# Optimization experiments

Hardware: AMD Instinct MI355X
Metric: run time of the kernel (lower is better)

## Reference

```python
import jax, jax.numpy as jnp
import numpy as np

N = 4096
FIN = 256
FOUT = 256
H = 1  # num_heads MUST be 1: edge projections reshape [N,N,H] -> (1,N,N)
NEG_MASK = -1000000.0
LRELU_SLOPE = 0.2
ESP = 1e-06
LN_EPS = 1e-05


def setup_inputs() -> dict:
    key = jax.random.key(0)
    ks = jax.random.split(key, 9)
    nodes_features = jax.random.normal(ks[0], (N, FIN), dtype=jnp.float32)
    degree_matrix = jax.random.normal(ks[1], (N, N), dtype=jnp.float32)
    edges_features_distance = jax.random.uniform(ks[2], (N, N), dtype=jnp.float32)
    edges_features_bond = jax.random.uniform(ks[3], (N, N), dtype=jnp.float32)
    # learned parameters (xavier-ish scale)
    proj_param = jax.random.normal(ks[4], (H, FIN, FOUT), dtype=jnp.float32) * (1.0 / np.sqrt(FIN))
    a_src = jax.random.normal(ks[5], (H, FOUT, 1), dtype=jnp.float32) * (1.0 / np.sqrt(FOUT))
    a_tgt = jax.random.normal(ks[6], (H, FOUT, 1), dtype=jnp.float32) * (1.0 / np.sqrt(FOUT))
    w_dist = jax.random.normal(ks[7], (H, 1), dtype=jnp.float32)  # nn.Linear(1, H).weight
    w_bond = jax.random.normal(ks[8], (H, 1), dtype=jnp.float32)
    return {
        "nodes_features": nodes_features,
        "degree_matrix": degree_matrix,
        "edges_features_distance": edges_features_distance,
        "edges_features_bond": edges_features_bond,
        "proj_param": proj_param,
        "a_src": a_src,
        "a_tgt": a_tgt,
        "w_dist": w_dist,
        "w_bond": w_bond,
        "cutoff": 0,
    }


def reference(nodes_features, degree_matrix, edges_features_distance,
              edges_features_bond, proj_param, a_src, a_tgt, w_dist, w_bond,
              cutoff=0):
    n = nodes_features.shape[0]
    h, fin, fout = proj_param.shape
    # connectivity mask: keep degree where positive, else large negative
    connectivity_mask = jnp.where(degree_matrix > 0, degree_matrix, NEG_MASK)
    # node projection: [H, N, Fout] (dropout is identity in eval)
    proj = jnp.einsum('nf,hfo->hno', nodes_features, proj_param)
    # attention scores: outer-sum of per-node source/target scores
    s_src = jnp.einsum('hno,hoi->hni', proj, a_src)      # [H, N, 1]
    s_tgt = jnp.einsum('hno,hoi->hni', proj, a_tgt)      # [H, N, 1]
    all_scores = jax.nn.leaky_relu(s_src + jnp.swapaxes(s_tgt, 1, 2), LRELU_SLOPE)  # [H,N,N]
    # edge contributions: Linear(1, H) on scalar edge features, reshaped (1,N,N) (H==1)
    dist_c = ((-edges_features_distance)[..., None] * w_dist[:, 0]).reshape(1, n, n)
    bond_c = (edges_features_bond[..., None] * w_bond[:, 0]).reshape(1, n, n)
    all_scores = all_scores + dist_c + bond_c
    # masked softmax over neighbors
    attn = jax.nn.softmax(all_scores + connectivity_mask[None], axis=-1)  # [H,N,N]
    # weighted aggregation
    out = jnp.einsum('hnm,hmo->hno', attn, proj)  # [H, N, Fout]
    # faithful to torch: transpose(2,1) -> [H,Fout,N] then contiguous view(-1,H,Fout)
    out = jnp.transpose(out, (0, 2, 1)).reshape(-1, h, fout)
    # concat heads (skip connection and bias are disabled per init args)
    out = out.reshape(-1, h * fout)
    out = jax.nn.elu(out)  # ELU activation, alpha=1
    # ---- no_grad connectivity update ----
    o = jax.lax.stop_gradient(out)
    dm = jax.lax.stop_gradient(degree_matrix)
    sim = o @ o.T                                        # [N, N]
    decay = -jax.lax.stop_gradient(edges_features_distance)
    upd = jax.nn.sigmoid(sim) * decay * (dm > 0).astype(o.dtype)
    upd = upd + ESP
    mean = jnp.mean(upd, axis=-1, keepdims=True)
    var = jnp.mean(jnp.square(upd - mean), axis=-1, keepdims=True)
    upd = (upd - mean) / jnp.sqrt(var + LN_EPS)          # layer_norm, no affine
    upd = upd + upd.T
    return out, upd
```

## Files before the change

kernel.cpp:

```cpp
#include <hip/hip_runtime.h>


using f32x4  = __attribute__((ext_vector_type(4))) float;
using bf16x8 = __attribute__((ext_vector_type(8))) __bf16;
using bf16x4 = __attribute__((ext_vector_type(4))) __bf16;
using u32x4  = __attribute__((ext_vector_type(4))) unsigned int;

__global__ __launch_bounds__(256) void cvt_nodes_kernel(const float* __restrict__ x,
                                                        __bf16* __restrict__ y) {
  int i = (blockIdx.x * 256 + threadIdx.x) * 4;
  f32x4 v = *(const f32x4*)(x + i);
  bf16x4 o = { (__bf16)v[0], (__bf16)v[1], (__bf16)v[2], (__bf16)v[3] };
  *(bf16x4*)(y + i) = o;
}

__global__ __launch_bounds__(256) void cvt_wt_kernel(const float* __restrict__ w,
                                                     __bf16* __restrict__ wt) {
  int i = blockIdx.x * 256 + threadIdx.x;
  int o = i >> 8, f = i & 255;
  wt[i] = (__bf16)w[f * 256 + o];
}

__global__ __launch_bounds__(256) void zero_kernel(float* __restrict__ p) {
  p[blockIdx.x * 256 + threadIdx.x] = 0.0f;
}

template<int BM, int BN, int MODE>
__global__ __launch_bounds__(256) void gemm_bf16_kernel(
    const __bf16* __restrict__ A, const __bf16* __restrict__ Bt,
    int M, int N, int K,
    float* __restrict__ outf, __bf16* __restrict__ outb,
    const float* __restrict__ e0, const float* __restrict__ e1,
    const __bf16* __restrict__ axp, float* __restrict__ outt)
{
  constexpr int LDT = 72;
  constexpr int MI = BM / 32;
  constexpr int NI = BN / 32;
  __shared__ alignas(16) __bf16 As[BM * LDT];
  __shared__ alignas(16) __bf16 Bs[BN * LDT];
  const int tid  = threadIdx.x;
  const int lane = tid & 63;
  const int wid  = tid >> 6;
  const int wm0  = (wid >> 1) * (BM / 2);
  const int wn0  = (wid & 1) * (BN / 2);
  const int m0   = blockIdx.x * BM;
  const int n0   = blockIdx.y * BN;
  const int lr   = lane & 15;
  const int lk   = lane >> 4;

  f32x4 acc[MI][NI];
#pragma unroll
  for (int a = 0; a < MI; ++a)
#pragma unroll
    for (int b = 0; b < NI; ++b) acc[a][b] = (f32x4){0.f, 0.f, 0.f, 0.f};

  for (int kt = 0; kt < K; kt += 64) {
    __syncthreads();
    for (int idx = tid; idx < BM * 8; idx += 256) {
      int r = idx >> 3, c = idx & 7;
      u32x4 v = *(const u32x4*)(A + (size_t)(m0 + r) * K + kt + c * 8);
      *(u32x4*)(As + r * LDT + c * 8) = v;
    }
    for (int idx = tid; idx < BN * 8; idx += 256) {
      int r = idx >> 3, c = idx & 7;
      u32x4 v = *(const u32x4*)(Bt + (size_t)(n0 + r) * K + kt + c * 8);
      *(u32x4*)(Bs + r * LDT + c * 8) = v;
    }
    __syncthreads();
#pragma unroll
    for (int kk = 0; kk < 2; ++kk) {
      bf16x8 av[MI], bv[NI];
#pragma unroll
      for (int mi = 0; mi < MI; ++mi)
        av[mi] = *(const bf16x8*)(As + (wm0 + mi * 16 + lr) * LDT + kk * 32 + lk * 8);
#pragma unroll
      for (int ni = 0; ni < NI; ++ni)
        bv[ni] = *(const bf16x8*)(Bs + (wn0 + ni * 16 + lr) * LDT + kk * 32 + lk * 8);
#pragma unroll
      for (int mi = 0; mi < MI; ++mi)
#pragma unroll
        for (int ni = 0; ni < NI; ++ni)
          acc[mi][ni] = __builtin_amdgcn_mfma_f32_16x16x32_bf16(av[mi], bv[ni], acc[mi][ni], 0, 0, 0);
    }
  }

#pragma unroll
  for (int mi = 0; mi < MI; ++mi) {
#pragma unroll
    for (int ni = 0; ni < NI; ++ni) {
#pragma unroll
      for (int j = 0; j < 4; ++j) {
        const int m = m0 + wm0 + mi * 16 + lk * 4 + j;
        const int n = n0 + wn0 + ni * 16 + lr;
        const float v = acc[mi][ni][j];
        if constexpr (MODE == 0) {
          outf[(size_t)m * 256 + n] = v;
          outb[(size_t)n * 4096 + m] = (__bf16)v;
        } else if constexpr (MODE == 2) {
          const size_t idx = (size_t)m * 4096 + n;
          const float d = e0[idx];
          const float g = e1[idx];
          const float s = 1.0f / (1.0f + expf(-v));
          outt[idx] = s * (-d) * (g > 0.f ? 1.0f : 0.0f) + 1e-6f;
        } else {
          const size_t idx = (size_t)m * 4096 + n;
          const float a = (float)axp[idx];
          const float s = 1.0f / (1.0f + expf(-v));
          outt[idx] = s * a + 1e-6f;
        }
      }
    }
  }
}

__global__ __launch_bounds__(256) void score_exp_kernel(
    const float* __restrict__ dist, const float* __restrict__ bond,
    const float* __restrict__ deg,  const float* __restrict__ ssrc,
    const float* __restrict__ stgt, const float* __restrict__ wdp,
    const float* __restrict__ wbp,  __bf16* __restrict__ P,
    __bf16* __restrict__ aux,       float* __restrict__ Lrow)
{
  const float wd = wdp[0], wb = wbp[0];
  const int lane = threadIdx.x & 63;
  size_t i = ((size_t)blockIdx.x * 256 + threadIdx.x) * 4;
  const size_t stride = (size_t)2048 * 256 * 4;
#pragma unroll 2
  for (int it = 0; it < 8; ++it, i += stride) {
    const int row = (int)(i >> 12);
    const int col = (int)(i & 4095);
    f32x4 d  = *(const f32x4*)(dist + i);
    f32x4 g  = *(const f32x4*)(deg + i);
    f32x4 b  = *(const f32x4*)(bond + i);
    f32x4 st = *(const f32x4*)(stgt + col);
    const float si = ssrc[row];
    f32x4 p;
    bf16x4 pb, ab;
#pragma unroll
    for (int q = 0; q < 4; ++q) {
      float x = si + st[q];
      x = x > 0.f ? x : 0.2f * x;
      x += -d[q] * wd + b[q] * wb + (g[q] > 0.f ? g[q] : -1000000.0f);
      p[q] = expf(x);
      pb[q] = (__bf16)p[q];
      ab[q] = (__bf16)(g[q] > 0.f ? -d[q] : 0.0f);
    }
    *(bf16x4*)(P + i) = pb;
    if (aux) *(bf16x4*)(aux + i) = ab;
    float s = p[0] + p[1] + p[2] + p[3];
#pragma unroll
    for (int o = 32; o; o >>= 1) s += __shfl_xor(s, o, 64);
    if (lane == 0) atomicAdd(Lrow + row, s);
  }
}

__global__ __launch_bounds__(256) void gemm_splitk_kernel(
    const __bf16* __restrict__ A, const __bf16* __restrict__ Bt,
    float* __restrict__ partial)
{
  constexpr int LDT = 72;
  __shared__ alignas(16) __bf16 As[64 * LDT];
  __shared__ alignas(16) __bf16 Bs[64 * LDT];
  const int tid  = threadIdx.x;
  const int lane = tid & 63;
  const int wid  = tid >> 6;
  const int wm0  = (wid >> 1) * 32;
  const int wn0  = (wid & 1) * 32;
  const int m0   = blockIdx.x * 64;
  const int n0   = blockIdx.y * 64;
  const int s    = blockIdx.z;
  const int lr   = lane & 15;
  const int lk   = lane >> 4;

  f32x4 acc[2][2];
#pragma unroll
  for (int a = 0; a < 2; ++a)
#pragma unroll
    for (int b = 0; b < 2; ++b) acc[a][b] = (f32x4){0.f, 0.f, 0.f, 0.f};

  const int k0 = s * 512;
  for (int kt = k0; kt < k0 + 512; kt += 64) {
    __syncthreads();
    for (int idx = tid; idx < 512; idx += 256) {
      int r = idx >> 3, c = idx & 7;
      u32x4 v = *(const u32x4*)(A + (size_t)(m0 + r) * 4096 + kt + c * 8);
      *(u32x4*)(As + r * LDT + c * 8) = v;
    }
    for (int idx = tid; idx < 512; idx += 256) {
      int r = idx >> 3, c = idx & 7;
      u32x4 v = *(const u32x4*)(Bt + (size_t)(n0 + r) * 4096 + kt + c * 8);
      *(u32x4*)(Bs + r * LDT + c * 8) = v;
    }
    __syncthreads();
#pragma unroll
    for (int kk = 0; kk < 2; ++kk) {
      bf16x8 av[2], bv[2];
#pragma unroll
      for (int mi = 0; mi < 2; ++mi)
        av[mi] = *(const bf16x8*)(As + (wm0 + mi * 16 + lr) * LDT + kk * 32 + lk * 8);
#pragma unroll
      for (int ni = 0; ni < 2; ++ni)
        bv[ni] = *(const bf16x8*)(Bs + (wn0 + ni * 16 + lr) * LDT + kk * 32 + lk * 8);
#pragma unroll
      for (int mi = 0; mi < 2; ++mi)
#pragma unroll
        for (int ni = 0; ni < 2; ++ni)
          acc[mi][ni] = __builtin_amdgcn_mfma_f32_16x16x32_bf16(av[mi], bv[ni], acc[mi][ni], 0, 0, 0);
    }
  }

  float* Pp = partial + (size_t)s * (4096 * 256);
#pragma unroll
  for (int mi = 0; mi < 2; ++mi)
#pragma unroll
    for (int ni = 0; ni < 2; ++ni)
#pragma unroll
      for (int j = 0; j < 4; ++j) {
        const int m = m0 + wm0 + mi * 16 + lk * 4 + j;
        const int n = n0 + wn0 + ni * 16 + lr;
        Pp[(size_t)m * 256 + n] = acc[mi][ni][j];
      }
}

__global__ __launch_bounds__(256) void reduce_elu_kernel(
    const float* __restrict__ partial, const float* __restrict__ Lrow,
    float* __restrict__ out0, __bf16* __restrict__ E)
{
  __shared__ float tile[64][65];
  __shared__ float invL[64];
  const int tid = threadIdx.x;
  const int m0 = blockIdx.x * 64;
  const int f0 = blockIdx.y * 64;
  if (tid < 64) invL[tid] = 1.0f / Lrow[m0 + tid];
  f32x4 accv[4];
#pragma unroll
  for (int i = 0; i < 4; ++i) {
    int lin = i * 1024 + tid * 4;
    int r = lin >> 6, c = lin & 63;
    f32x4 sum = (f32x4){0.f, 0.f, 0.f, 0.f};
#pragma unroll
    for (int s = 0; s < 8; ++s)
      sum += *(const f32x4*)(partial + (size_t)s * (4096 * 256) +
                             (size_t)(m0 + r) * 256 + f0 + c);
    accv[i] = sum;
  }
  __syncthreads();
#pragma unroll
  for (int i = 0; i < 4; ++i) {
    int lin = i * 1024 + tid * 4;
    int r = lin >> 6, c = lin & 63;
    const float inv = invL[r];
    tile[r][c]     = accv[i][0] * inv;
    tile[r][c + 1] = accv[i][1] * inv;
    tile[r][c + 2] = accv[i][2] * inv;
    tile[r][c + 3] = accv[i][3] * inv;
  }
  __syncthreads();
#pragma unroll
  for (int i = 0; i < 4; ++i) {
    int lin = i * 1024 + tid * 4;
    int rr = lin >> 6, cc = lin & 63;
    f32x4 e;
#pragma unroll
    for (int q = 0; q < 4; ++q) {
      float v = tile[cc + q][rr];
      e[q] = v > 0.f ? v : expm1f(v);
    }
    size_t idx = (size_t)(f0 + rr) * 4096 + m0 + cc;
    *(f32x4*)(out0 + idx) = e;
    bf16x4 eb = { (__bf16)e[0], (__bf16)e[1], (__bf16)e[2], (__bf16)e[3] };
    *(bf16x4*)(E + idx) = eb;
  }
}

__global__ __launch_bounds__(256) void sproj_kernel(const float* __restrict__ proj,
                                                    const float* __restrict__ asrc,
                                                    const float* __restrict__ atgt,
                                                    float* __restrict__ ssrc,
                                                    float* __restrict__ stgt) {
  const int row  = blockIdx.x * 4 + (threadIdx.x >> 6);
  const int lane = threadIdx.x & 63;
  f32x4 p = *(const f32x4*)(proj + (size_t)row * 256 + lane * 4);
  f32x4 a = *(const f32x4*)(asrc + lane * 4);
  f32x4 b = *(const f32x4*)(atgt + lane * 4);
  float d1 = p[0]*a[0] + p[1]*a[1] + p[2]*a[2] + p[3]*a[3];
  float d2 = p[0]*b[0] + p[1]*b[1] + p[2]*b[2] + p[3]*b[3];
#pragma unroll
  for (int o = 32; o; o >>= 1) { d1 += __shfl_xor(d1, o, 64); d2 += __shfl_xor(d2, o, 64); }
  if (lane == 0) { ssrc[row] = d1; stgt[row] = d2; }
}

__global__ __launch_bounds__(256, 4) void stats_kernel(const float* __restrict__ t,
                                                       float* __restrict__ mean,
                                                       float* __restrict__ rstd) {
  const int row = blockIdx.x;
  const int tid = threadIdx.x;
  const float* tr = t + (size_t)row * 4096;
  f32x4 v[4];
#pragma unroll
  for (int u = 0; u < 4; ++u) v[u] = *(const f32x4*)(tr + u * 1024 + tid * 4);
  float s = 0.f, s2 = 0.f;
#pragma unroll
  for (int u = 0; u < 4; ++u)
#pragma unroll
    for (int q = 0; q < 4; ++q) { s += v[u][q]; s2 += v[u][q] * v[u][q]; }
#pragma unroll
  for (int o = 32; o; o >>= 1) { s += __shfl_xor(s, o, 64); s2 += __shfl_xor(s2, o, 64); }
  __shared__ float bs[4], bs2[4];
  if ((tid & 63) == 0) { bs[tid >> 6] = s; bs2[tid >> 6] = s2; }
  __syncthreads();
  if (tid == 0) {
    float S  = bs[0] + bs[1] + bs[2] + bs[3];
    float S2 = bs2[0] + bs2[1] + bs2[2] + bs2[3];
    float m  = S * (1.0f / 4096.0f);
    float var = S2 * (1.0f / 4096.0f) - m * m;
    mean[row] = m;
    rstd[row] = rsqrtf(var + 1e-5f);
  }
}

__global__ __launch_bounds__(256) void finalize_kernel(float* __restrict__ t,
                                                       const float* __restrict__ mean,
                                                       const float* __restrict__ rstd) {
  const int bj = blockIdx.x, bi = blockIdx.y;
  if (bi > bj) return;
  __shared__ float ta[64][65];
  __shared__ float tb[64][65];
  const int tid = threadIdx.x;
#pragma unroll
  for (int i = 0; i < 4; ++i) {
    int lin = i * 1024 + tid * 4;
    int r = lin >> 6, c = lin & 63;
    f32x4 va = *(const f32x4*)(t + (size_t)(bi * 64 + r) * 4096 + bj * 64 + c);
    ta[r][c] = va[0]; ta[r][c+1] = va[1]; ta[r][c+2] = va[2]; ta[r][c+3] = va[3];
  }
  if (bi != bj) {
#pragma unroll
    for (int i = 0; i < 4; ++i) {
      int lin = i * 1024 + tid * 4;
      int r = lin >> 6, c = lin & 63;
      f32x4 vb = *(const f32x4*)(t + (size_t)(bj * 64 + r) * 4096 + bi * 64 + c);
      tb[r][c] = vb[0]; tb[r][c+1] = vb[1]; tb[r][c+2] = vb[2]; tb[r][c+3] = vb[3];
    }
  }
  __syncthreads();
#pragma unroll
  for (int i = 0; i < 4; ++i) {
    int lin = i * 1024 + tid * 4;
    int r = lin >> 6, c = lin & 63;
    int gi = bi * 64 + r, gj = bj * 64 + c;
    const float mi_ = mean[gi], ri_ = rstd[gi];
    f32x4 mj = *(const f32x4*)(mean + gj);
    f32x4 rj = *(const f32x4*)(rstd + gj);
    f32x4 o;
#pragma unroll
    for (int q = 0; q < 4; ++q) {
      float v = (ta[r][c + q] - mi_) * ri_;
      float w = (bi == bj) ? (ta[c + q][r] - mj[q]) * rj[q]
                           : (tb[c + q][r] - mj[q]) * rj[q];
      o[q] = v + w;
    }
    *(f32x4*)(t + (size_t)gi * 4096 + gj) = o;
  }
  if (bi != bj) {
#pragma unroll
    for (int i = 0; i < 4; ++i) {
      int lin = i * 1024 + tid * 4;
      int r = lin >> 6, c = lin & 63;
      int gi = bj * 64 + r, gj = bi * 64 + c;
      const float mi_ = mean[gi], ri_ = rstd[gi];
      f32x4 mj = *(const f32x4*)(mean + gj);
      f32x4 rj = *(const f32x4*)(rstd + gj);
      f32x4 o;
#pragma unroll
      for (int q = 0; q < 4; ++q) {
        float v = (tb[r][c + q] - mi_) * ri_;
        float w = (ta[c + q][r] - mj[q]) * rj[q];
        o[q] = v + w;
      }
      *(f32x4*)(t + (size_t)gi * 4096 + gj) = o;
    }
  }
}

extern "C" void kernel_launch(void* const* d_in, const int* in_sizes, int n_in,
                              void* d_out, int out_size, void* d_ws, size_t ws_size,
                              hipStream_t stream) {
  const float* nodes  = (const float*)d_in[0];
  const float* degree = (const float*)d_in[1];
  const float* dist   = (const float*)d_in[2];
  const float* bond   = (const float*)d_in[3];
  const float* W      = (const float*)d_in[4];
  const float* a_src  = (const float*)d_in[5];
  const float* a_tgt  = (const float*)d_in[6];
  const float* w_dist = (const float*)d_in[7];
  const float* w_bond = (const float*)d_in[8];

  char* ws = (char*)d_ws;
  __bf16* nodesB = (__bf16*)ws;
  __bf16* Wt     = (__bf16*)(ws + (2u << 20));
  __bf16* projT  = (__bf16*)(ws + (2u << 20) + (256u << 10));
  float*  proj   = (float*)(ws + (5u << 20));
  float*  ssrc   = (float*)(ws + (11u << 20));
  float*  stgt   = ssrc + 4096;
  float*  mean   = stgt + 4096;
  float*  rstd   = mean + 4096;
  float*  Lrow   = rstd + 4096;

  const bool useAux = ws_size >= (size_t)(44u << 20);
  __bf16* aux = useAux ? (__bf16*)(ws + (12u << 20)) : nullptr;

  float*  out0 = (float*)d_out;
  float*  t    = out0 + (size_t)4096 * 256;
  __bf16* P    = (__bf16*)t;
  float*  partials = t + (size_t)4096 * 4096 / 2;
  __bf16* E    = (__bf16*)(ws + (9u << 20));

  cvt_nodes_kernel<<<1024, 256, 0, stream>>>(nodes, nodesB);
  cvt_wt_kernel<<<256, 256, 0, stream>>>(W, Wt);

  gemm_bf16_kernel<64, 64, 0><<<dim3(64, 4), 256, 0, stream>>>(
      nodesB, Wt, 4096, 256, 256, proj, projT, nullptr, nullptr, nullptr, nullptr);

  sproj_kernel<<<1024, 256, 0, stream>>>(proj, a_src, a_tgt, ssrc, stgt);

  zero_kernel<<<16, 256, 0, stream>>>(Lrow);

  score_exp_kernel<<<2048, 256, 0, stream>>>(dist, bond, degree, ssrc, stgt,
                                             w_dist, w_bond, P, aux, Lrow);

  gemm_splitk_kernel<<<dim3(64, 4, 8), 256, 0, stream>>>(P, projT, partials);

  reduce_elu_kernel<<<dim3(64, 4), 256, 0, stream>>>(partials, Lrow, out0, E);

  if (useAux)
    gemm_bf16_kernel<128, 128, 3><<<dim3(32, 32), 256, 0, stream>>>(
        E, E, 4096, 4096, 256, nullptr, nullptr, nullptr, nullptr, aux, t);
  else
    gemm_bf16_kernel<128, 128, 2><<<dim3(32, 32), 256, 0, stream>>>(
        E, E, 4096, 4096, 256, nullptr, nullptr, dist, degree, nullptr, t);

  stats_kernel<<<4096, 256, 0, stream>>>(t, mean, rstd);

  finalize_kernel<<<dim3(64, 64), 256, 0, stream>>>(t, mean, rstd);
}
```

Baseline: 184.7 us.

## Replace atomic row sums with rowsum kernel, store split-K partials in bf16

```diff
diff --git a/kernel.cpp b/kernel.cpp
--- a/kernel.cpp
+++ b/kernel.cpp
@@ -19,10 +19,6 @@
   int i = blockIdx.x * 256 + threadIdx.x;
   int o = i >> 8, f = i & 255;
   wt[i] = (__bf16)w[f * 256 + o];
-}
-
-__global__ __launch_bounds__(256) void zero_kernel(float* __restrict__ p) {
-  p[blockIdx.x * 256 + threadIdx.x] = 0.0f;
 }
 
 template<int BM, int BN, int MODE>
@@ -100,12 +96,12 @@
           const size_t idx = (size_t)m * 4096 + n;
           const float d = e0[idx];
           const float g = e1[idx];
-          const float s = 1.0f / (1.0f + expf(-v));
+          const float s = 1.0f / (1.0f + __expf(-v));
           outt[idx] = s * (-d) * (g > 0.f ? 1.0f : 0.0f) + 1e-6f;
         } else {
           const size_t idx = (size_t)m * 4096 + n;
           const float a = (float)axp[idx];
-          const float s = 1.0f / (1.0f + expf(-v));
+          const float s = 1.0f / (1.0f + __expf(-v));
           outt[idx] = s * a + 1e-6f;
         }
       }
@@ -118,13 +114,12 @@
     const float* __restrict__ deg,  const float* __restrict__ ssrc,
     const float* __restrict__ stgt, const float* __restrict__ wdp,
     const float* __restrict__ wbp,  __bf16* __restrict__ P,
-    __bf16* __restrict__ aux,       float* __restrict__ Lrow)
+    __bf16* __restrict__ aux)
 {
   const float wd = wdp[0], wb = wbp[0];
-  const int lane = threadIdx.x & 63;
   size_t i = ((size_t)blockIdx.x * 256 + threadIdx.x) * 4;
   const size_t stride = (size_t)2048 * 256 * 4;
-#pragma unroll 2
+#pragma unroll 4
   for (int it = 0; it < 8; ++it, i += stride) {
     const int row = (int)(i >> 12);
     const int col = (int)(i & 4095);
@@ -133,29 +128,40 @@
     f32x4 b  = *(const f32x4*)(bond + i);
     f32x4 st = *(const f32x4*)(stgt + col);
     const float si = ssrc[row];
-    f32x4 p;
     bf16x4 pb, ab;
 #pragma unroll
     for (int q = 0; q < 4; ++q) {
       float x = si + st[q];
       x = x > 0.f ? x : 0.2f * x;
       x += -d[q] * wd + b[q] * wb + (g[q] > 0.f ? g[q] : -1000000.0f);
-      p[q] = expf(x);
-      pb[q] = (__bf16)p[q];
+      pb[q] = (__bf16)__expf(x);
       ab[q] = (__bf16)(g[q] > 0.f ? -d[q] : 0.0f);
     }
     *(bf16x4*)(P + i) = pb;
     if (aux) *(bf16x4*)(aux + i) = ab;
-    float s = p[0] + p[1] + p[2] + p[3];
-#pragma unroll
-    for (int o = 32; o; o >>= 1) s += __shfl_xor(s, o, 64);
-    if (lane == 0) atomicAdd(Lrow + row, s);
-  }
+  }
+}
+
+__global__ __launch_bounds__(256) void rowsum_kernel(const __bf16* __restrict__ P,
+                                                     float* __restrict__ Lrow) {
+  const int row  = blockIdx.x * 4 + (threadIdx.x >> 6);
+  const int lane = threadIdx.x & 63;
+  const __bf16* pr = P + (size_t)row * 4096;
+  float s = 0.f;
+#pragma unroll
+  for (int u = 0; u < 8; ++u) {
+    bf16x8 v = *(const bf16x8*)(pr + u * 512 + lane * 8);
+#pragma unroll
+    for (int q = 0; q < 8; ++q) s += (float)v[q];
+  }
+#pragma unroll
+  for (int o = 32; o; o >>= 1) s += __shfl_xor(s, o, 64);
+  if (lane == 0) Lrow[row] = s;
 }
 
 __global__ __launch_bounds__(256) void gemm_splitk_kernel(
     const __bf16* __restrict__ A, const __bf16* __restrict__ Bt,
-    float* __restrict__ partial)
+    __bf16* __restrict__ partial)
 {
   constexpr int LDT = 72;
   __shared__ alignas(16) __bf16 As[64 * LDT];
@@ -208,7 +214,7 @@
     }
   }
 
-  float* Pp = partial + (size_t)s * (4096 * 256);
+  __bf16* Pp = partial + (size_t)s * (4096 * 256);
 #pragma unroll
   for (int mi = 0; mi < 2; ++mi)
 #pragma unroll
@@ -217,12 +223,12 @@
       for (int j = 0; j < 4; ++j) {
         const int m = m0 + wm0 + mi * 16 + lk * 4 + j;
         const int n = n0 + wn0 + ni * 16 + lr;
-        Pp[(size_t)m * 256 + n] = acc[mi][ni][j];
+        Pp[(size_t)m * 256 + n] = (__bf16)acc[mi][ni][j];
       }
 }
 
 __global__ __launch_bounds__(256) void reduce_elu_kernel(
-    const float* __restrict__ partial, const float* __restrict__ Lrow,
+    const __bf16* __restrict__ partial, const float* __restrict__ Lrow,
     float* __restrict__ out0, __bf16* __restrict__ E)
 {
   __shared__ float tile[64][65];
@@ -238,9 +244,12 @@
     int r = lin >> 6, c = lin & 63;
     f32x4 sum = (f32x4){0.f, 0.f, 0.f, 0.f};
 #pragma unroll
-    for (int s = 0; s < 8; ++s)
-      sum += *(const f32x4*)(partial + (size_t)s * (4096 * 256) +
-                             (size_t)(m0 + r) * 256 + f0 + c);
+    for (int s = 0; s < 8; ++s) {
+      bf16x4 pv = *(const bf16x4*)(partial + (size_t)s * (4096 * 256) +
+                                   (size_t)(m0 + r) * 256 + f0 + c);
+#pragma unroll
+      for (int q = 0; q < 4; ++q) sum[q] += (float)pv[q];
+    }
     accv[i] = sum;
   }
   __syncthreads();
@@ -400,6 +409,7 @@
   __bf16* Wt     = (__bf16*)(ws + (2u << 20));
   __bf16* projT  = (__bf16*)(ws + (2u << 20) + (256u << 10));
   float*  proj   = (float*)(ws + (5u << 20));
+  __bf16* E      = (__bf16*)(ws + (9u << 20));
   float*  ssrc   = (float*)(ws + (11u << 20));
   float*  stgt   = ssrc + 4096;
   float*  mean   = stgt + 4096;
@@ -412,8 +422,7 @@
   float*  out0 = (float*)d_out;
   float*  t    = out0 + (size_t)4096 * 256;
   __bf16* P    = (__bf16*)t;
-  float*  partials = t + (size_t)4096 * 4096 / 2;
-  __bf16* E    = (__bf16*)(ws + (9u << 20));
+  __bf16* partials = (__bf16*)((char*)t + ((size_t)32 << 20));
 
   cvt_nodes_kernel<<<1024, 256, 0, stream>>>(nodes, nodesB);
   cvt_wt_kernel<<<256, 256, 0, stream>>>(W, Wt);
@@ -423,10 +432,10 @@
 
   sproj_kernel<<<1024, 256, 0, stream>>>(proj, a_src, a_tgt, ssrc, stgt);
 
-  zero_kernel<<<16, 256, 0, stream>>>(Lrow);
-
   score_exp_kernel<<<2048, 256, 0, stream>>>(dist, bond, degree, ssrc, stgt,
-                                             w_dist, w_bond, P, aux, Lrow);
+                                             w_dist, w_bond, P, aux);
+
+  rowsum_kernel<<<1024, 256, 0, stream>>>(P, Lrow);
 
   gemm_splitk_kernel<<<dim3(64, 4, 8), 256, 0, stream>>>(P, projT, partials);
 
```

Measured after the change: 177.8 us. 3.7% less time.
